# Kernel optimization log

Hardware: AMD Instinct MI355X
Metric: run time of the kernel (lower is better)

The kernel has to match this reference:

```python
import jax, jax.numpy as jnp
import numpy as np


def setup_inputs() -> dict:
    key = jax.random.key(0)
    ks = jax.random.split(key, 8)
    B = 32768
    return {
        "x": jax.random.normal(ks[0], (B, 784), dtype=jnp.float32),
        "conv_w": jax.random.normal(ks[1], (3, 3), dtype=jnp.float32),
        "fc1_w": jax.random.normal(ks[2], (512, 676), dtype=jnp.float32) * 0.04,
        "fc1_b": jax.random.normal(ks[3], (512,), dtype=jnp.float32),
        "fc2_w": jax.random.normal(ks[4], (512, 512), dtype=jnp.float32) * 0.04,
        "fc2_b": jax.random.normal(ks[5], (512,), dtype=jnp.float32),
        "out_w": jax.random.normal(ks[6], (10, 512), dtype=jnp.float32) * 0.04,
        "out_b": jax.random.normal(ks[7], (10,), dtype=jnp.float32),
    }


def reference(x, conv_w, fc1_w, fc1_b, fc2_w, fc2_b, out_w, out_b):
    B = x.shape[0]
    img = x.reshape(B, 1, 28, 28)  # NCHW, single channel
    # Valid 3x3 cross-correlation (same math as the nested tensordot loop).
    kern = conv_w.reshape(1, 1, 3, 3)  # OIHW
    conv = jax.lax.conv_general_dilated(
        img, kern, window_strides=(1, 1), padding="VALID",
        dimension_numbers=("NCHW", "OIHW", "NCHW"))  # [B,1,26,26]
    h = conv.reshape(B, 26 * 26)
    h = jax.nn.relu(h @ fc1_w.T + fc1_b)
    h = jax.nn.relu(h @ fc2_w.T + fc2_b)
    return h @ out_w.T + out_b  # [B,10] logits
```

## Files before the change

kernel.cpp:

```cpp
#include <hip/hip_runtime.h>

typedef unsigned short ushort_t;
typedef __attribute__((ext_vector_type(8))) short bf16x8;
typedef __attribute__((ext_vector_type(4))) float f32x4;

__device__ __forceinline__ unsigned short f2bf(float f) {
    union { float f; unsigned u; } v; v.f = f;
    unsigned r = v.u + 0x7FFFu + ((v.u >> 16) & 1u);
    return (unsigned short)(r >> 16);
}

__device__ __forceinline__ void gl_lds16(const void* g, void* l) {
    __builtin_amdgcn_global_load_lds(
        (const __attribute__((address_space(1))) unsigned int*)g,
        (__attribute__((address_space(3))) unsigned int*)l, 16, 0, 0);
}

__global__ __launch_bounds__(256) void prep_w1eff(const float* __restrict__ fc1_w,
                                                  const float* __restrict__ cw,
                                                  ushort_t* __restrict__ W1) {
    int idx = blockIdx.x * 256 + threadIdx.x;
    if (idx >= 512 * 832) return;
    int n = idx / 832, p = idx % 832;
    float acc = 0.f;
    if (p < 784) {
        int pr = p / 28, pc = p % 28;
#pragma unroll
        for (int dr = 0; dr < 3; ++dr) {
            int r = pr - dr;
            if (r < 0 || r >= 26) continue;
#pragma unroll
            for (int dc = 0; dc < 3; ++dc) {
                int col = pc - dc;
                if (col < 0 || col >= 26) continue;
                acc += cw[dr * 3 + dc] * fc1_w[n * 676 + r * 26 + col];
            }
        }
    }
    W1[idx] = f2bf(acc);
}

__global__ __launch_bounds__(256) void prep_w2(const float* __restrict__ w, ushort_t* __restrict__ W2) {
    int idx = blockIdx.x * 256 + threadIdx.x;
    W2[idx] = f2bf(w[idx]);
}
__global__ __launch_bounds__(256) void prep_w3(const float* __restrict__ w, ushort_t* __restrict__ W3) {
    int idx = blockIdx.x * 256 + threadIdx.x;
    if (idx >= 16 * 512) return;
    W3[idx] = (idx < 10 * 512) ? f2bf(w[idx]) : (ushort_t)0;
}

__global__ __launch_bounds__(256) void cast_x(const float* __restrict__ x, ushort_t* __restrict__ Xb) {
    int idx = blockIdx.x * 256 + threadIdx.x;
    int m = idx / 208, j = idx % 208;
    if (m >= 32768) return;
    uint2 pack;
    if (j < 196) {
        const float4 v = *(const float4*)&x[(size_t)m * 784 + j * 4];
        pack.x = (unsigned)f2bf(v.x) | ((unsigned)f2bf(v.y) << 16);
        pack.y = (unsigned)f2bf(v.z) | ((unsigned)f2bf(v.w) << 16);
    } else {
        pack.x = 0; pack.y = 0;
    }
    *(uint2*)&Xb[(size_t)m * 832 + j * 4] = pack;
}

template <int LDA, int KSTEPS, bool RELU>
__global__ __launch_bounds__(256) void gemm_bias_act(const ushort_t* __restrict__ A,
                                                     const ushort_t* __restrict__ W,
                                                     const float* __restrict__ bias,
                                                     ushort_t* __restrict__ C) {
    __shared__ ushort_t As[128 * 64];
    __shared__ ushort_t Bs[128 * 64];
    const int tid = threadIdx.x;
    const int wave = tid >> 6, lane = tid & 63;
    const int m0 = blockIdx.x * 128, n0 = blockIdx.y * 128;
    const int srow = lane >> 3;
    const int sseg = lane & 7;
    const int gseg = sseg ^ (srow & 7);
    const int wm = wave >> 1, wn = wave & 1;
    const int quad = lane >> 4, l16 = lane & 15;
    f32x4 acc[4][4] = {};

    for (int ks = 0; ks < KSTEPS; ++ks) {
        const int k0 = ks * 64;
#pragma unroll
        for (int t = 0; t < 4; ++t) {
            const int r0 = wave * 32 + t * 8;
            const int row = r0 + srow;
            gl_lds16(A + (size_t)(m0 + row) * LDA + k0 + gseg * 8, &As[r0 * 64]);
            gl_lds16(W + (size_t)(n0 + row) * LDA + k0 + gseg * 8, &Bs[r0 * 64]);
        }
        __syncthreads();
#pragma unroll
        for (int kk = 0; kk < 2; ++kk) {
            const int q = kk * 4 + quad;
            bf16x8 af[4], bfr[4];
#pragma unroll
            for (int i = 0; i < 4; ++i) {
                const int mr = wm * 64 + i * 16 + l16;
                af[i] = *(const bf16x8*)&As[mr * 64 + ((q ^ (mr & 7)) * 8)];
                const int nr = wn * 64 + i * 16 + l16;
                bfr[i] = *(const bf16x8*)&Bs[nr * 64 + ((q ^ (nr & 7)) * 8)];
            }
#pragma unroll
            for (int i = 0; i < 4; ++i)
#pragma unroll
                for (int j = 0; j < 4; ++j)
                    acc[i][j] = __builtin_amdgcn_mfma_f32_16x16x32_bf16(af[i], bfr[j], acc[i][j], 0, 0, 0);
        }
        __syncthreads();
    }

#pragma unroll
    for (int j = 0; j < 4; ++j) {
        const int n = n0 + wn * 64 + j * 16 + l16;
        const float bb = bias[n];
#pragma unroll
        for (int i = 0; i < 4; ++i) {
            const int mb = m0 + wm * 64 + i * 16 + quad * 4;
#pragma unroll
            for (int r = 0; r < 4; ++r) {
                float v = acc[i][j][r] + bb;
                if (RELU) v = fmaxf(v, 0.0f);
                C[(size_t)(mb + r) * 512 + n] = f2bf(v);
            }
        }
    }
}

__global__ __launch_bounds__(256) void head_gemm(const ushort_t* __restrict__ h2,
                                                 const ushort_t* __restrict__ W3,
                                                 const float* __restrict__ ob,
                                                 float* __restrict__ out) {
    __shared__ ushort_t Bs[16 * 520];
    const int tid = threadIdx.x;
    for (int i = tid; i < 16 * 512; i += 256)
        Bs[(i >> 9) * 520 + (i & 511)] = W3[i];
    __syncthreads();
    const int wave = tid >> 6, lane = tid & 63;
    const int quad = lane >> 4, l16 = lane & 15;
    const int m0 = blockIdx.x * 64 + wave * 16;
    f32x4 acc = {0.f, 0.f, 0.f, 0.f};
#pragma unroll
    for (int ks = 0; ks < 16; ++ks) {
        bf16x8 a = *(const bf16x8*)&h2[(size_t)(m0 + l16) * 512 + ks * 32 + quad * 8];
        bf16x8 b = *(const bf16x8*)&Bs[l16 * 520 + ks * 32 + quad * 8];
        acc = __builtin_amdgcn_mfma_f32_16x16x32_bf16(a, b, acc, 0, 0, 0);
    }
    if (l16 < 10) {
        const float bb = ob[l16];
#pragma unroll
        for (int r = 0; r < 4; ++r)
            out[(size_t)(m0 + quad * 4 + r) * 10 + l16] = acc[r] + bb;
    }
}

extern "C" void kernel_launch(void* const* d_in, const int* in_sizes, int n_in,
                              void* d_out, int out_size, void* d_ws, size_t ws_size,
                              hipStream_t stream) {
    const float* x      = (const float*)d_in[0];
    const float* conv_w = (const float*)d_in[1];
    const float* fc1_w  = (const float*)d_in[2];
    const float* fc1_b  = (const float*)d_in[3];
    const float* fc2_w  = (const float*)d_in[4];
    const float* fc2_b  = (const float*)d_in[5];
    const float* out_w  = (const float*)d_in[6];
    const float* out_b  = (const float*)d_in[7];
    float* out = (float*)d_out;

    ushort_t* W1 = (ushort_t*)d_ws;
    ushort_t* W2 = W1 + 512 * 832;
    ushort_t* W3 = W2 + 512 * 512;
    ushort_t* Xb = W3 + 16 * 512;
    ushort_t* h1 = Xb + (size_t)32768 * 832;
    ushort_t* h2 = Xb;

    prep_w1eff<<<dim3((512 * 832 + 255) / 256), 256, 0, stream>>>(fc1_w, conv_w, W1);
    prep_w2<<<dim3((512 * 512) / 256), 256, 0, stream>>>(fc2_w, W2);
    prep_w3<<<dim3(32), 256, 0, stream>>>(out_w, W3);

    cast_x<<<dim3((32768 * 208 + 255) / 256), 256, 0, stream>>>(x, Xb);

    gemm_bias_act<832, 13, true><<<dim3(256, 4), 256, 0, stream>>>(Xb, W1, fc1_b, h1);
    gemm_bias_act<512, 8,  true><<<dim3(256, 4), 256, 0, stream>>>(h1, W2, fc2_b, h2);

    head_gemm<<<dim3(512), 256, 0, stream>>>(h2, W3, out_b, out);
}
```

Measured before the change: 251.3 us.

## Use 32x32x16 MFMA in GEMMs, merge weight prep kernels, stage head rows in LDS

```diff
diff --git a/kernel.cpp b/kernel.cpp
--- a/kernel.cpp
+++ b/kernel.cpp
@@ -3,6 +3,7 @@
 typedef unsigned short ushort_t;
 typedef __attribute__((ext_vector_type(8))) short bf16x8;
 typedef __attribute__((ext_vector_type(4))) float f32x4;
+typedef __attribute__((ext_vector_type(16))) float f32x16;
 
 __device__ __forceinline__ unsigned short f2bf(float f) {
     union { float f; unsigned u; } v; v.f = f;
@@ -16,38 +17,35 @@
         (__attribute__((address_space(3))) unsigned int*)l, 16, 0, 0);
 }
 
-__global__ __launch_bounds__(256) void prep_w1eff(const float* __restrict__ fc1_w,
-                                                  const float* __restrict__ cw,
-                                                  ushort_t* __restrict__ W1) {
+__global__ __launch_bounds__(256) void prep_all(const float* __restrict__ fc1_w,
+                                                const float* __restrict__ cw,
+                                                const float* __restrict__ fc2_w,
+                                                const float* __restrict__ out_w,
+                                                ushort_t* __restrict__ W1,
+                                                ushort_t* __restrict__ W2,
+                                                ushort_t* __restrict__ W3) {
     int idx = blockIdx.x * 256 + threadIdx.x;
-    if (idx >= 512 * 832) return;
-    int n = idx / 832, p = idx % 832;
-    float acc = 0.f;
-    if (p < 784) {
-        int pr = p / 28, pc = p % 28;
+    if (idx < 512 * 832) {
+        int n = idx / 832, p = idx % 832;
+        float acc = 0.f;
+        if (p < 784) {
+            int pr = p / 28, pc = p % 28;
 #pragma unroll
-        for (int dr = 0; dr < 3; ++dr) {
-            int r = pr - dr;
-            if (r < 0 || r >= 26) continue;
+            for (int dr = 0; dr < 3; ++dr) {
+                int r = pr - dr;
+                if (r < 0 || r >= 26) continue;
 #pragma unroll
-            for (int dc = 0; dc < 3; ++dc) {
-                int col = pc - dc;
-                if (col < 0 || col >= 26) continue;
-                acc += cw[dr * 3 + dc] * fc1_w[n * 676 + r * 26 + col];
+                for (int dc = 0; dc < 3; ++dc) {
+                    int col = pc - dc;
+                    if (col < 0 || col >= 26) continue;
+                    acc += cw[dr * 3 + dc] * fc1_w[n * 676 + r * 26 + col];
+                }
             }
         }
+        W1[idx] = f2bf(acc);
     }
-    W1[idx] = f2bf(acc);
-}
-
-__global__ __launch_bounds__(256) void prep_w2(const float* __restrict__ w, ushort_t* __restrict__ W2) {
-    int idx = blockIdx.x * 256 + threadIdx.x;
-    W2[idx] = f2bf(w[idx]);
-}
-__global__ __launch_bounds__(256) void prep_w3(const float* __restrict__ w, ushort_t* __restrict__ W3) {
-    int idx = blockIdx.x * 256 + threadIdx.x;
-    if (idx >= 16 * 512) return;
-    W3[idx] = (idx < 10 * 512) ? f2bf(w[idx]) : (ushort_t)0;
+    if (idx < 512 * 512) W2[idx] = f2bf(fc2_w[idx]);
+    if (idx < 16 * 512)  W3[idx] = (idx < 10 * 512) ? f2bf(out_w[idx]) : (ushort_t)0;
 }
 
 __global__ __launch_bounds__(256) void cast_x(const float* __restrict__ x, ushort_t* __restrict__ Xb) {
@@ -79,8 +77,8 @@
     const int sseg = lane & 7;
     const int gseg = sseg ^ (srow & 7);
     const int wm = wave >> 1, wn = wave & 1;
-    const int quad = lane >> 4, l16 = lane & 15;
-    f32x4 acc[4][4] = {};
+    const int r32 = lane & 31, half = lane >> 5;
+    f32x16 acc[2][2] = {};
 
     for (int ks = 0; ks < KSTEPS; ++ks) {
         const int k0 = ks * 64;
@@ -93,37 +91,38 @@
         }
         __syncthreads();
 #pragma unroll
-        for (int kk = 0; kk < 2; ++kk) {
-            const int q = kk * 4 + quad;
-            bf16x8 af[4], bfr[4];
+        for (int ksub = 0; ksub < 4; ++ksub) {
+            const int q = ksub * 2 + half;
+            bf16x8 af[2], bfr[2];
 #pragma unroll
-            for (int i = 0; i < 4; ++i) {
-                const int mr = wm * 64 + i * 16 + l16;
+            for (int i = 0; i < 2; ++i) {
+                const int mr = wm * 64 + i * 32 + r32;
                 af[i] = *(const bf16x8*)&As[mr * 64 + ((q ^ (mr & 7)) * 8)];
-                const int nr = wn * 64 + i * 16 + l16;
+                const int nr = wn * 64 + i * 32 + r32;
                 bfr[i] = *(const bf16x8*)&Bs[nr * 64 + ((q ^ (nr & 7)) * 8)];
             }
 #pragma unroll
-            for (int i = 0; i < 4; ++i)
+            for (int i = 0; i < 2; ++i)
 #pragma unroll
-                for (int j = 0; j < 4; ++j)
-                    acc[i][j] = __builtin_amdgcn_mfma_f32_16x16x32_bf16(af[i], bfr[j], acc[i][j], 0, 0, 0);
+                for (int j = 0; j < 2; ++j)
+                    acc[i][j] = __builtin_amdgcn_mfma_f32_32x32x16_bf16(af[i], bfr[j], acc[i][j], 0, 0, 0);
         }
         __syncthreads();
     }
 
 #pragma unroll
-    for (int j = 0; j < 4; ++j) {
-        const int n = n0 + wn * 64 + j * 16 + l16;
+    for (int j = 0; j < 2; ++j) {
+        const int n = n0 + wn * 64 + j * 32 + r32;
         const float bb = bias[n];
 #pragma unroll
-        for (int i = 0; i < 4; ++i) {
-            const int mb = m0 + wm * 64 + i * 16 + quad * 4;
+        for (int i = 0; i < 2; ++i) {
+            const int mbase = m0 + wm * 64 + i * 32 + 4 * half;
 #pragma unroll
-            for (int r = 0; r < 4; ++r) {
-                float v = acc[i][j][r] + bb;
+            for (int reg = 0; reg < 16; ++reg) {
+                const int row = mbase + (reg & 3) + 8 * (reg >> 2);
+                float v = acc[i][j][reg] + bb;
                 if (RELU) v = fmaxf(v, 0.0f);
-                C[(size_t)(mb + r) * 512 + n] = f2bf(v);
+                C[(size_t)row * 512 + n] = f2bf(v);
             }
         }
     }
@@ -133,26 +132,26 @@
                                                  const ushort_t* __restrict__ W3,
                                                  const float* __restrict__ ob,
                                                  float* __restrict__ out) {
-    __shared__ ushort_t Bs[16 * 520];
+    __shared__ ushort_t Hs[64 * 520];
     const int tid = threadIdx.x;
-    for (int i = tid; i < 16 * 512; i += 256)
-        Bs[(i >> 9) * 520 + (i & 511)] = W3[i];
+    const int wave = tid >> 6, lane = tid & 63;
+    const int m0 = blockIdx.x * 64;
+    for (int r = wave; r < 64; r += 4)
+        gl_lds16(h2 + (size_t)(m0 + r) * 512 + lane * 8, &Hs[r * 520]);
     __syncthreads();
-    const int wave = tid >> 6, lane = tid & 63;
     const int quad = lane >> 4, l16 = lane & 15;
-    const int m0 = blockIdx.x * 64 + wave * 16;
     f32x4 acc = {0.f, 0.f, 0.f, 0.f};
 #pragma unroll
     for (int ks = 0; ks < 16; ++ks) {
-        bf16x8 a = *(const bf16x8*)&h2[(size_t)(m0 + l16) * 512 + ks * 32 + quad * 8];
-        bf16x8 b = *(const bf16x8*)&Bs[l16 * 520 + ks * 32 + quad * 8];
+        bf16x8 a = *(const bf16x8*)&Hs[(wave * 16 + l16) * 520 + ks * 32 + quad * 8];
+        bf16x8 b = *(const bf16x8*)&W3[l16 * 512 + ks * 32 + quad * 8];
         acc = __builtin_amdgcn_mfma_f32_16x16x32_bf16(a, b, acc, 0, 0, 0);
     }
     if (l16 < 10) {
         const float bb = ob[l16];
 #pragma unroll
         for (int r = 0; r < 4; ++r)
-            out[(size_t)(m0 + quad * 4 + r) * 10 + l16] = acc[r] + bb;
+            out[(size_t)(m0 + wave * 16 + quad * 4 + r) * 10 + l16] = acc[r] + bb;
     }
 }
 
@@ -176,9 +175,7 @@
     ushort_t* h1 = Xb + (size_t)32768 * 832;
     ushort_t* h2 = Xb;
 
-    prep_w1eff<<<dim3((512 * 832 + 255) / 256), 256, 0, stream>>>(fc1_w, conv_w, W1);
-    prep_w2<<<dim3((512 * 512) / 256), 256, 0, stream>>>(fc2_w, W2);
-    prep_w3<<<dim3(32), 256, 0, stream>>>(out_w, W3);
+    prep_all<<<dim3((512 * 832 + 255) / 256), 256, 0, stream>>>(fc1_w, conv_w, fc2_w, out_w, W1, W2, W3);
 
     cast_x<<<dim3((32768 * 208 + 255) / 256), 256, 0, stream>>>(x, Xb);
 
```

Result: no change. 249.9 us (-0.6%).
